# Performance work log

Hardware: AMD Instinct MI355X
Metric: run time of the kernel (lower is better)

The kernel has to match this reference:

```python
import jax, jax.numpy as jnp
import numpy as np

B, S, D, H = 4, 2048, 1024, 16
DEPTH = D // H


def setup_inputs() -> dict:
    key = jax.random.key(0)
    ks = jax.random.split(key, 12)
    q = jax.random.normal(ks[0], (B, S, D), dtype=jnp.float32)
    k = jax.random.normal(ks[1], (B, S, D), dtype=jnp.float32)
    v = jax.random.normal(ks[2], (B, S, D), dtype=jnp.float32)
    # causal mask: 1.0 where attention is disallowed (upper triangle), per `mask * -1e9`
    mask = 1.0 - jnp.tril(jnp.ones((S, S), dtype=jnp.float32))
    mask = mask[None, None, :, :]  # [1,1,S,S] broadcastable over batch/heads
    scale = 1.0 / np.sqrt(D)
    Wq = jax.random.normal(ks[3], (D, D), dtype=jnp.float32) * scale
    Wk = jax.random.normal(ks[4], (D, D), dtype=jnp.float32) * scale
    Wv = jax.random.normal(ks[5], (D, D), dtype=jnp.float32) * scale
    Wo = jax.random.normal(ks[6], (D, D), dtype=jnp.float32) * scale
    bq = jnp.zeros((D,), jnp.float32)
    bk = jnp.zeros((D,), jnp.float32)
    bv = jnp.zeros((D,), jnp.float32)
    bo = jnp.zeros((D,), jnp.float32)
    return {"query": q, "key": k, "value": v, "mask": mask,
            "Wq": Wq, "bq": bq, "Wk": Wk, "bk": bk,
            "Wv": Wv, "bv": bv, "Wo": Wo, "bo": bo}


def _split_heads(x):
    # [B, S, D] -> [B, H, S, depth]
    b, s, _ = x.shape
    return x.reshape(b, s, H, DEPTH).transpose(0, 2, 1, 3)


def reference(query, key, value, mask, Wq, bq, Wk, bk, Wv, bv, Wo, bo):
    q = _split_heads(query @ Wq + bq)   # [B,H,S,depth]
    k = _split_heads(key @ Wk + bk)
    v = _split_heads(value @ Wv + bv)
    scores = jnp.einsum('bhqd,bhkd->bhqk', q, k) / jnp.sqrt(
        jnp.asarray(DEPTH, q.dtype))
    scores = scores + mask * (-1e9)
    attn = jax.nn.softmax(scores, axis=-1)
    out = jnp.einsum('bhqk,bhkd->bhqd', attn, v)   # [B,H,S,depth]
    out = out.transpose(0, 2, 1, 3).reshape(query.shape[0], -1, H * DEPTH)
    return out @ Wo + bo
```

## Files before the change

kernel.cpp:

```cpp
#include <hip/hip_runtime.h>

#define Bsz 4
#define SEQ 2048
#define DIM 1024
#define NH 16
#define HD 64

typedef float  f32x4  __attribute__((ext_vector_type(4)));
typedef __bf16 bf16x8 __attribute__((ext_vector_type(8)));
typedef __bf16 bf16x4 __attribute__((ext_vector_type(4)));
typedef short  s16x4  __attribute__((ext_vector_type(4)));

__device__ __forceinline__ f32x4 mfma16(bf16x8 a, bf16x8 b, f32x4 c) {
    return __builtin_amdgcn_mfma_f32_16x16x32_bf16(a, b, c, 0, 0, 0);
}
__device__ __forceinline__ f32x4 mfma16k16(bf16x4 a, bf16x4 b, f32x4 c) {
#if defined(__has_builtin) && __has_builtin(__builtin_amdgcn_mfma_f32_16x16x16bf16_1k)
    return __builtin_amdgcn_mfma_f32_16x16x16bf16_1k(
        __builtin_bit_cast(s16x4, a), __builtin_bit_cast(s16x4, b), c, 0, 0, 0);
#else
    asm volatile("s_nop 2\n\tv_mfma_f32_16x16x16_bf16 %0, %1, %2, %0\n\ts_nop 7\n\ts_nop 7"
                 : "+v"(c) : "v"(a), "v"(b));
    return c;
#endif
}

#define GLD_LDS16(gsrc, ldst)                                                        \
    __builtin_amdgcn_global_load_lds(                                                \
        (const __attribute__((address_space(1))) void*)(gsrc),                       \
        (__attribute__((address_space(3))) void*)(ldst), 16, 0, 0)

__global__ __launch_bounds__(256) void cvt_kernel(
    const float* __restrict__ x0, const float* __restrict__ x1,
    const float* __restrict__ x2,
    __bf16* __restrict__ o0, __bf16* __restrict__ o1, __bf16* __restrict__ o2)
{
    int z = blockIdx.y;
    const float* X = (z == 0) ? x0 : (z == 1) ? x1 : x2;
    __bf16*      O = (z == 0) ? o0 : (z == 1) ? o1 : o2;
    size_t i = ((size_t)blockIdx.x * 256 + threadIdx.x) * 8;
    f32x4 a = *(const f32x4*)(X + i);
    f32x4 b = *(const f32x4*)(X + i + 4);
    bf16x8 r;
#pragma unroll
    for (int j = 0; j < 4; j++) { r[j] = (__bf16)a[j]; r[4 + j] = (__bf16)b[j]; }
    *(bf16x8*)(O + i) = r;
}

__global__ __launch_bounds__(256) void wt_kernel(
    const float* __restrict__ Wq, const float* __restrict__ Wk,
    const float* __restrict__ Wv, const float* __restrict__ Wo,
    __bf16* __restrict__ wt)
{
    __shared__ float tile[64][65];
    int z = blockIdx.z;
    const float* W = (z == 0) ? Wq : (z == 1) ? Wk : (z == 2) ? Wv : Wo;
    __bf16* out = wt + (size_t)z * DIM * DIM;
    int kb = blockIdx.x * 64, nb = blockIdx.y * 64;
    int t = threadIdx.x;
    int cidx = t & 63, ridx = t >> 6;
#pragma unroll
    for (int i = 0; i < 16; i++) {
        int r = ridx + i * 4;
        tile[r][cidx] = W[(size_t)(kb + r) * DIM + nb + cidx];
    }
    __syncthreads();
#pragma unroll
    for (int i = 0; i < 16; i++) {
        int r = ridx + i * 4;
        out[(size_t)(nb + r) * DIM + kb + cidx] = (__bf16)tile[cidx][r];
    }
}

__global__ __launch_bounds__(256, 2) void gemm_proj(
    const __bf16* __restrict__ Xq, const __bf16* __restrict__ Xk,
    const __bf16* __restrict__ Xv, const __bf16* __restrict__ wt,
    const float* __restrict__ bq, const float* __restrict__ bk,
    const float* __restrict__ bv,
    __bf16* __restrict__ oq, __bf16* __restrict__ ok, __bf16* __restrict__ ovT)
{
    int z = blockIdx.z;
    const __bf16* X    = (z == 0) ? Xq : (z == 1) ? Xk : Xv;
    const float*  bias = (z == 0) ? bq : (z == 1) ? bk : bv;
    const __bf16* Bt   = wt + (size_t)z * DIM * DIM;

    __shared__ __align__(16) char smem[32768];
    __bf16* const Ab = (__bf16*)smem;
    __bf16* const Bb = (__bf16*)(smem + 16384);

    int m0 = blockIdx.x * 128, n0 = blockIdx.y * 128;
    int tid = threadIdx.x, lane = tid & 63, w = tid >> 6;
    int c = lane & 15, g = lane >> 4;
    int wm = (w >> 1) * 64, wn = (w & 1) * 64;

    f32x4 acc[4][4] = {};

    int srow = (w * 2) * 16 + (lane >> 2);
    int scol = (lane & 3) * 8;
    const __bf16* aptr0 = X + (size_t)(m0 + srow) * DIM + scol;
    const __bf16* aptr1 = aptr0 + (size_t)16 * DIM;
    const __bf16* bptr0 = Bt + (size_t)(n0 + srow) * DIM + scol;
    const __bf16* bptr1 = bptr0 + (size_t)16 * DIM;
    int so0 = (w * 2) * 512;
    int so1 = (w * 2 + 1) * 512;

    GLD_LDS16(aptr0, Ab + so0);
    GLD_LDS16(aptr1, Ab + so1);
    GLD_LDS16(bptr0, Bb + so0);
    GLD_LDS16(bptr1, Bb + so1);
    __syncthreads();

    int cur = 0;
    for (int kt = 0; kt < 32; ++kt) {
        int nxt = kt + 1;
        int nb = cur ^ 1;
        if (nxt < 32) {
            int k0 = nxt * 32;
            GLD_LDS16(aptr0 + k0, Ab + nb * 4096 + so0);
            GLD_LDS16(aptr1 + k0, Ab + nb * 4096 + so1);
            GLD_LDS16(bptr0 + k0, Bb + nb * 4096 + so0);
            GLD_LDS16(bptr1 + k0, Bb + nb * 4096 + so1);
        }
        bf16x8 af[4], bf[4];
#pragma unroll
        for (int mf = 0; mf < 4; mf++)
            af[mf] = *(bf16x8*)&Ab[cur * 4096 + (wm + mf * 16 + c) * 32 + g * 8];
#pragma unroll
        for (int nf = 0; nf < 4; nf++)
            bf[nf] = *(bf16x8*)&Bb[cur * 4096 + (wn + nf * 16 + c) * 32 + g * 8];
#pragma unroll
        for (int mf = 0; mf < 4; mf++)
#pragma unroll
            for (int nf = 0; nf < 4; nf++)
                acc[mf][nf] = mfma16(af[mf], bf[nf], acc[mf][nf]);
        __syncthreads();
        cur = nb;
    }

    if (z == 2) {
        __bf16* T = (__bf16*)smem + (size_t)w * 2304;
        int h = (n0 + wn) >> 6;
        int bb = m0 >> 11;
        int s_base = (m0 & (SEQ - 1)) + wm;
        int dd = lane >> 2;
        int ss = (lane & 3) * 8;
        size_t obase = ((size_t)(bb * NH + h) * HD) * SEQ;
#pragma unroll
        for (int half = 0; half < 2; half++) {
#pragma unroll
            for (int mh = 0; mh < 2; mh++) {
                int mf = half * 2 + mh;
#pragma unroll
                for (int nf = 0; nf < 4; nf++) {
                    int col = n0 + wn + nf * 16 + c;
                    int d = nf * 16 + c;
                    float bval = bias[col];
                    bf16x4 pk;
#pragma unroll
                    for (int r = 0; r < 4; r++) pk[r] = (__bf16)(acc[mf][nf][r] + bval);
                    *(bf16x4*)&T[d * 36 + mh * 16 + g * 4] = pk;
                }
            }
#pragma unroll
            for (int dgrp = 0; dgrp < 4; dgrp++) {
                int d = dgrp * 16 + dd;
                bf16x8 vv = *(bf16x8*)&T[d * 36 + ss];
                *(bf16x8*)&ovT[obase + (size_t)d * SEQ + s_base + half * 32 + ss] = vv;
            }
        }
    } else {
        __bf16* Out = (z == 0) ? oq : ok;
#pragma unroll
        for (int nf = 0; nf < 4; nf++) {
            int col = n0 + wn + nf * 16 + c;
            float bval = bias[col];
#pragma unroll
            for (int mf = 0; mf < 4; mf++) {
                int row = m0 + wm + mf * 16 + g * 4;
#pragma unroll
                for (int r = 0; r < 4; r++)
                    Out[(size_t)(row + r) * DIM + col] = (__bf16)(acc[mf][nf][r] + bval);
            }
        }
    }
}

__global__ __launch_bounds__(256, 2) void gemm_proj_f32(
    const float* __restrict__ Xq, const float* __restrict__ Xk,
    const float* __restrict__ Xv, const __bf16* __restrict__ wt,
    const float* __restrict__ bq, const float* __restrict__ bk,
    const float* __restrict__ bv,
    __bf16* __restrict__ oq, __bf16* __restrict__ ok, __bf16* __restrict__ ovT)
{
    int z = blockIdx.z;
    const float*  X    = (z == 0) ? Xq : (z == 1) ? Xk : Xv;
    const float*  bias = (z == 0) ? bq : (z == 1) ? bk : bv;
    const __bf16* Bt   = wt + (size_t)z * DIM * DIM;

    __shared__ __align__(16) char smem[36864];
    __bf16* const Ab = (__bf16*)smem;
    __bf16* const Bb = (__bf16*)(smem + 16384);

    int m0 = blockIdx.x * 128, n0 = blockIdx.y * 128;
    int tid = threadIdx.x, lane = tid & 63, w = tid >> 6;
    int c = lane & 15, g = lane >> 4;
    int wm = (w >> 1) * 64, wn = (w & 1) * 64;

    f32x4 acc[4][4] = {};

    int ar = tid >> 1, ah = tid & 1;
    const float* aptr = X + (size_t)(m0 + ar) * DIM + ah * 16;
    int awo = ar * 32 + ah * 16;

    int brow0 = (w * 2) * 16 + (lane >> 2);
    int bcol  = (lane & 3) * 8;
    const __bf16* bptr0 = Bt + (size_t)(n0 + brow0) * DIM + bcol;
    const __bf16* bptr1 = bptr0 + (size_t)16 * DIM;
    int bwo0 = (w * 2) * 512;
    int bwo1 = (w * 2 + 1) * 512;

    {
        f32x4 f0 = *(const f32x4*)(aptr);
        f32x4 f1 = *(const f32x4*)(aptr + 4);
        f32x4 f2 = *(const f32x4*)(aptr + 8);
        f32x4 f3 = *(const f32x4*)(aptr + 12);
        GLD_LDS16(bptr0, Bb + bwo0);
        GLD_LDS16(bptr1, Bb + bwo1);
        bf16x8 b0, b1;
#pragma unroll
        for (int j = 0; j < 4; j++) {
            b0[j] = (__bf16)f0[j]; b0[4 + j] = (__bf16)f1[j];
            b1[j] = (__bf16)f2[j]; b1[4 + j] = (__bf16)f3[j];
        }
        *(bf16x8*)(Ab + awo)     = b0;
        *(bf16x8*)(Ab + awo + 8) = b1;
    }
    __syncthreads();

    int cur = 0;
    for (int kt = 0; kt < 32; ++kt) {
        int nxt = kt + 1;
        int nb = cur ^ 1;
        f32x4 f0, f1, f2, f3;
        if (nxt < 32) {
            const float* ap = aptr + nxt * 32;
            f0 = *(const f32x4*)(ap);
            f1 = *(const f32x4*)(ap + 4);
            f2 = *(const f32x4*)(ap + 8);
            f3 = *(const f32x4*)(ap + 12);
            GLD_LDS16(bptr0 + nxt * 32, Bb + nb * 4096 + bwo0);
            GLD_LDS16(bptr1 + nxt * 32, Bb + nb * 4096 + bwo1);
        }
        bf16x8 af[4], bf[4];
#pragma unroll
        for (int mf = 0; mf < 4; mf++)
            af[mf] = *(bf16x8*)&Ab[cur * 4096 + (wm + mf * 16 + c) * 32 + g * 8];
#pragma unroll
        for (int nf = 0; nf < 4; nf++)
            bf[nf] = *(bf16x8*)&Bb[cur * 4096 + (wn + nf * 16 + c) * 32 + g * 8];
#pragma unroll
        for (int mf = 0; mf < 4; mf++)
#pragma unroll
            for (int nf = 0; nf < 4; nf++)
                acc[mf][nf] = mfma16(af[mf], bf[nf], acc[mf][nf]);
        if (nxt < 32) {
            bf16x8 b0, b1;
#pragma unroll
            for (int j = 0; j < 4; j++) {
                b0[j] = (__bf16)f0[j]; b0[4 + j] = (__bf16)f1[j];
                b1[j] = (__bf16)f2[j]; b1[4 + j] = (__bf16)f3[j];
            }
            *(bf16x8*)(Ab + nb * 4096 + awo)     = b0;
            *(bf16x8*)(Ab + nb * 4096 + awo + 8) = b1;
        }
        __syncthreads();
        cur = nb;
    }

    if (z == 2) {
        __bf16* T = (__bf16*)smem + (size_t)w * 4608;
#pragma unroll
        for (int nf = 0; nf < 4; nf++) {
            int col = n0 + wn + nf * 16 + c;
            int d = nf * 16 + c;
            float bval = bias[col];
#pragma unroll
            for (int mf = 0; mf < 4; mf++) {
                int sl = mf * 16 + g * 4;
                bf16x4 pk;
#pragma unroll
                for (int r = 0; r < 4; r++) pk[r] = (__bf16)(acc[mf][nf][r] + bval);
                *(bf16x4*)&T[d * 72 + sl] = pk;
            }
        }
        int h = (n0 + wn) >> 6;
        int bb = m0 >> 11;
        int s_base = (m0 & (SEQ - 1)) + wm;
        int dd = lane >> 2;
        int ss = (lane & 3) * 8;
        size_t obase = ((size_t)(bb * NH + h) * HD) * SEQ;
#pragma unroll
        for (int dgrp = 0; dgrp < 4; dgrp++)
#pragma unroll
            for (int half = 0; half < 2; half++) {
                int d = dgrp * 16 + dd;
                int s = half * 32 + ss;
                bf16x8 vv = *(bf16x8*)&T[d * 72 + s];
                *(bf16x8*)&ovT[obase + (size_t)d * SEQ + s_base + s] = vv;
            }
    } else {
        __bf16* Out = (z == 0) ? oq : ok;
#pragma unroll
        for (int nf = 0; nf < 4; nf++) {
            int col = n0 + wn + nf * 16 + c;
            float bval = bias[col];
#pragma unroll
            for (int mf = 0; mf < 4; mf++) {
                int row = m0 + wm + mf * 16 + g * 4;
#pragma unroll
                for (int r = 0; r < 4; r++)
                    Out[(size_t)(row + r) * DIM + col] = (__bf16)(acc[mf][nf][r] + bval);
            }
        }
    }
}

#define QSCALE 0.180336880f

__global__ __launch_bounds__(256, 2) void fa_kernel(
    const __bf16* __restrict__ qp, const __bf16* __restrict__ kp,
    const __bf16* __restrict__ vpT, __bf16* __restrict__ op)
{
    int bz = blockIdx.x;
    int bh = bz & 63;
    int b = bh >> 4, h = bh & 15;
    int qt = 15 - (bz >> 6);
    int q0 = qt * 128;

    int tid = threadIdx.x, lane = tid & 63, w = tid >> 6;
    int c = lane & 15, g = lane >> 4;

    __shared__ __bf16 Kbuf[64 * 64];
    __shared__ __bf16 Vbuf[64 * 64];

    const int qb[2] = {q0 + w * 16, q0 + 64 + w * 16};

    bf16x8 qf[2][2];
#pragma unroll
    for (int nq = 0; nq < 2; nq++) {
        const __bf16* qbase = qp + (size_t)(b * SEQ + qb[nq] + c) * DIM + h * HD;
#pragma unroll
        for (int kc = 0; kc < 2; kc++) {
            bf16x8 raw = *(const bf16x8*)(qbase + kc * 32 + g * 8);
            bf16x8 sc;
#pragma unroll
            for (int j = 0; j < 8; j++) sc[j] = (__bf16)((float)raw[j] * QSCALE);
            qf[nq][kc] = sc;
        }
    }

    f32x4 acc[4][2] = {};
    float m_run[2] = {-1e30f, -1e30f};
    float l_run[2] = {0.f, 0.f};

    int r8 = tid >> 3, c8 = tid & 7;
    int sch = c8 ^ (r8 & 7);
    const __bf16* kbase = kp  + (size_t)(b * SEQ + r8) * DIM + h * HD + sch * 8;
    const __bf16* vbase = vpT + ((size_t)(b * NH + h) * HD + r8) * SEQ + sch * 8;
    __bf16* kdst0 = Kbuf + w * 512;
    __bf16* kdst1 = Kbuf + 2048 + w * 512;
    __bf16* vdst0 = Vbuf + w * 512;
    __bf16* vdst1 = Vbuf + 2048 + w * 512;

    int vb4[4];
#pragma unroll
    for (int mkey = 0; mkey < 4; mkey++)
        vb4[mkey] = c * 64 + (((2 * mkey + (g >> 1)) ^ (c & 7)) * 8) + (g & 1) * 4;

    int ktmax = (q0 >> 6) + 2;
    for (int kt = 0; kt < ktmax; ++kt) {
        GLD_LDS16(kbase + (size_t)kt * 64 * DIM, kdst0);
        GLD_LDS16(kbase + (size_t)(kt * 64 + 32) * DIM, kdst1);
        GLD_LDS16(vbase + kt * 64, vdst0);
        GLD_LDS16(vbase + kt * 64 + (size_t)32 * SEQ, vdst1);
        __syncthreads();

        bool need0 = (kt * 64 <= qb[0] + 15);
        int kb0 = kt * 64;

        f32x4 s[4][2] = {};
#pragma unroll
        for (int kc = 0; kc < 2; kc++) {
            bf16x8 kf[4];
#pragma unroll
            for (int mkey = 0; mkey < 4; mkey++)
                kf[mkey] = *(bf16x8*)&Kbuf[(mkey * 16 + c) * 64 + (((kc * 4 + g) ^ (c & 7)) * 8)];
#pragma unroll
            for (int mkey = 0; mkey < 4; mkey++) {
                if (need0) s[mkey][0] = mfma16(kf[mkey], qf[0][kc], s[mkey][0]);
                s[mkey][1] = mfma16(kf[mkey], qf[1][kc], s[mkey][1]);
            }
        }

        bf16x4 pf[4][2];
#pragma unroll
        for (int nq = 0; nq < 2; nq++) {
            if (nq == 0 && !need0) continue;
            int qg = qb[nq] + c;
            if (kb0 + 63 > qg) {
#pragma unroll
                for (int mkey = 0; mkey < 4; mkey++)
#pragma unroll
                    for (int r2 = 0; r2 < 4; r2++)
                        if (kb0 + mkey * 16 + g * 4 + r2 > qg) s[mkey][nq][r2] = -1e30f;
            }
            float pm0 = fmaxf(fmaxf(s[0][nq][0], s[0][nq][1]), fmaxf(s[0][nq][2], s[0][nq][3]));
            float pm1 = fmaxf(fmaxf(s[1][nq][0], s[1][nq][1]), fmaxf(s[1][nq][2], s[1][nq][3]));
            float pm2 = fmaxf(fmaxf(s[2][nq][0], s[2][nq][1]), fmaxf(s[2][nq][2], s[2][nq][3]));
            float pm3 = fmaxf(fmaxf(s[3][nq][0], s[3][nq][1]), fmaxf(s[3][nq][2], s[3][nq][3]));
            float pm = fmaxf(fmaxf(pm0, pm1), fmaxf(pm2, pm3));
            pm = fmaxf(pm, __shfl_xor(pm, 16));
            pm = fmaxf(pm, __shfl_xor(pm, 32));
            float mo = m_run[nq];
            float mn = fmaxf(mo, pm);
            m_run[nq] = mn;
            float scl = exp2f(mo - mn);
            l_run[nq] *= scl;
#pragma unroll
            for (int nf = 0; nf < 4; nf++) acc[nf][nq] *= scl;
            float rs = 0.f;
#pragma unroll
            for (int mkey = 0; mkey < 4; mkey++) {
                bf16x4 pk;
#pragma unroll
                for (int r2 = 0; r2 < 4; r2++) {
                    float p = exp2f(s[mkey][nq][r2] - mn);
                    rs += p;
                    pk[r2] = (__bf16)p;
                }
                pf[mkey][nq] = pk;
            }
            rs += __shfl_xor(rs, 16);
            rs += __shfl_xor(rs, 32);
            l_run[nq] += rs;
        }

#pragma unroll
        for (int mkey = 0; mkey < 4; mkey++) {
#pragma unroll
            for (int nf = 0; nf < 4; nf++) {
                bf16x4 vf = *(bf16x4*)&Vbuf[vb4[mkey] + nf * 1024];
                if (need0) acc[nf][0] = mfma16k16(vf, pf[mkey][0], acc[nf][0]);
                acc[nf][1] = mfma16k16(vf, pf[mkey][1], acc[nf][1]);
            }
        }
        __syncthreads();
    }

#pragma unroll
    for (int nq = 0; nq < 2; nq++) {
        float inv = 1.f / l_run[nq];
        int row = qb[nq] + c;
        __bf16* obase = op + (size_t)(b * SEQ + row) * DIM + h * HD + g * 4;
#pragma unroll
        for (int nf = 0; nf < 4; nf++) {
            bf16x4 pk;
#pragma unroll
            for (int r2 = 0; r2 < 4; r2++) pk[r2] = (__bf16)(acc[nf][nq][r2] * inv);
            *(bf16x4*)(obase + nf * 16) = pk;
        }
    }
}

__global__ __launch_bounds__(256, 2) void gemm_out(
    const __bf16* __restrict__ Ain, const __bf16* __restrict__ wt,
    const float* __restrict__ bias, float* __restrict__ Out)
{
    const __bf16* Bt = wt + (size_t)3 * DIM * DIM;

    __shared__ __bf16 Ab[2][4096];
    __shared__ __bf16 Bb[2][4096];

    int m0 = blockIdx.x * 128, n0 = blockIdx.y * 128;
    int tid = threadIdx.x, lane = tid & 63, w = tid >> 6;
    int c = lane & 15, g = lane >> 4;
    int wm = (w >> 1) * 64, wn = (w & 1) * 64;

    f32x4 acc[4][4] = {};

    int srow = (w * 2) * 16 + (lane >> 2);
    int scol = (lane & 3) * 8;
    const __bf16* aptr0 = Ain + (size_t)(m0 + srow) * DIM + scol;
    const __bf16* aptr1 = aptr0 + (size_t)16 * DIM;
    const __bf16* bptr0 = Bt + (size_t)(n0 + srow) * DIM + scol;
    const __bf16* bptr1 = bptr0 + (size_t)16 * DIM;
    int so0 = (w * 2) * 512;
    int so1 = (w * 2 + 1) * 512;

    GLD_LDS16(aptr0, Ab[0] + so0);
    GLD_LDS16(aptr1, Ab[0] + so1);
    GLD_LDS16(bptr0, Bb[0] + so0);
    GLD_LDS16(bptr1, Bb[0] + so1);
    __syncthreads();

    int cur = 0;
    for (int kt = 0; kt < 32; ++kt) {
        int nxt = kt + 1;
        int nb = cur ^ 1;
        if (nxt < 32) {
            int k0 = nxt * 32;
            GLD_LDS16(aptr0 + k0, Ab[nb] + so0);
            GLD_LDS16(aptr1 + k0, Ab[nb] + so1);
            GLD_LDS16(bptr0 + k0, Bb[nb] + so0);
            GLD_LDS16(bptr1 + k0, Bb[nb] + so1);
        }
        bf16x8 af[4], bf[4];
#pragma unroll
        for (int mf = 0; mf < 4; mf++)
            af[mf] = *(bf16x8*)&Ab[cur][(wm + mf * 16 + c) * 32 + g * 8];
#pragma unroll
        for (int nf = 0; nf < 4; nf++)
            bf[nf] = *(bf16x8*)&Bb[cur][(wn + nf * 16 + c) * 32 + g * 8];
#pragma unroll
        for (int mf = 0; mf < 4; mf++)
#pragma unroll
            for (int nf = 0; nf < 4; nf++)
                acc[mf][nf] = mfma16(af[mf], bf[nf], acc[mf][nf]);
        __syncthreads();
        cur = nb;
    }

#pragma unroll
    for (int nf = 0; nf < 4; nf++) {
        int col = n0 + wn + nf * 16 + c;
        float bval = bias[col];
#pragma unroll
        for (int mf = 0; mf < 4; mf++) {
            int row = m0 + wm + mf * 16 + g * 4;
#pragma unroll
            for (int r = 0; r < 4; r++)
                Out[(size_t)(row + r) * DIM + col] = acc[mf][nf][r] + bval;
        }
    }
}

extern "C" void kernel_launch(void* const* d_in, const int* in_sizes, int n_in,
                              void* d_out, int out_size, void* d_ws, size_t ws_size,
                              hipStream_t stream)
{
    const float* q  = (const float*)d_in[0];
    const float* k  = (const float*)d_in[1];
    const float* v  = (const float*)d_in[2];
    const float* Wq = (const float*)d_in[4];
    const float* bq = (const float*)d_in[5];
    const float* Wk = (const float*)d_in[6];
    const float* bk = (const float*)d_in[7];
    const float* Wv = (const float*)d_in[8];
    const float* bv = (const float*)d_in[9];
    const float* Wo = (const float*)d_in[10];
    const float* bo = (const float*)d_in[11];

    char* ws = (char*)d_ws;
    __bf16* wt  = (__bf16*)ws;
    __bf16* qp  = (__bf16*)(ws + (size_t)(8u  << 20));
    __bf16* kp  = (__bf16*)(ws + (size_t)(24u << 20));
    __bf16* vpT = (__bf16*)(ws + (size_t)(40u << 20));
    __bf16* ao  = (__bf16*)(ws + (size_t)(56u << 20));
    __bf16* xq  = (__bf16*)(ws + (size_t)(72u << 20));
    __bf16* xk  = (__bf16*)(ws + (size_t)(88u << 20));
    __bf16* xv  = (__bf16*)(ws + (size_t)(104u << 20));

    wt_kernel<<<dim3(16, 16, 4), 256, 0, stream>>>(Wq, Wk, Wv, Wo, wt);
    if (ws_size >= ((size_t)120u << 20)) {
        cvt_kernel<<<dim3(4096, 3), 256, 0, stream>>>(q, k, v, xq, xk, xv);
        gemm_proj<<<dim3(64, 8, 3), 256, 0, stream>>>(xq, xk, xv, wt, bq, bk, bv, qp, kp, vpT);
    } else {
        gemm_proj_f32<<<dim3(64, 8, 3), 256, 0, stream>>>(q, k, v, wt, bq, bk, bv, qp, kp, vpT);
    }
    fa_kernel<<<dim3(1024), 256, 0, stream>>>(qp, kp, vpT, ao);
    gemm_out<<<dim3(64, 8), 256, 0, stream>>>(ao, wt, bo, (float*)d_out);

    (void)in_sizes; (void)n_in; (void)out_size;
}
```

Baseline: 203.5 us.

## Halve flash-attention query tile to 64 rows and add lazy softmax rescaling

Each attention block now handles 64 query rows (one 16-row strip per wave) instead of 128, and the grid doubles to 2048 blocks. This gives more parallelism and finer causal load balance, and drops the need0 branching, at the cost of loading each K/V tile twice as often per query row. It also adds a lazy rescale: the running max and accumulator rescale are updated only when some lane's new max exceeds the old one by more than 8 in log2 space. That skips exp and multiply work on most iterations, but it lets unnormalised probabilities grow up to 2^8.

```diff
diff --git a/kernel.cpp b/kernel.cpp
--- a/kernel.cpp
+++ b/kernel.cpp
@@ -334,8 +334,8 @@
     int bz = blockIdx.x;
     int bh = bz & 63;
     int b = bh >> 4, h = bh & 15;
-    int qt = 15 - (bz >> 6);
-    int q0 = qt * 128;
+    int qt = 31 - (bz >> 6);
+    int q0 = qt * 64;
 
     int tid = threadIdx.x, lane = tid & 63, w = tid >> 6;
     int c = lane & 15, g = lane >> 4;
@@ -343,25 +343,25 @@
     __shared__ __bf16 Kbuf[64 * 64];
     __shared__ __bf16 Vbuf[64 * 64];
 
-    const int qb[2] = {q0 + w * 16, q0 + 64 + w * 16};
-
-    bf16x8 qf[2][2];
-#pragma unroll
-    for (int nq = 0; nq < 2; nq++) {
-        const __bf16* qbase = qp + (size_t)(b * SEQ + qb[nq] + c) * DIM + h * HD;
+    const int qb = q0 + w * 16;
+    const int qg = qb + c;
+
+    bf16x8 qf[2];
+    {
+        const __bf16* qbase = qp + (size_t)(b * SEQ + qg) * DIM + h * HD;
 #pragma unroll
         for (int kc = 0; kc < 2; kc++) {
             bf16x8 raw = *(const bf16x8*)(qbase + kc * 32 + g * 8);
             bf16x8 sc;
 #pragma unroll
             for (int j = 0; j < 8; j++) sc[j] = (__bf16)((float)raw[j] * QSCALE);
-            qf[nq][kc] = sc;
-        }
-    }
-
-    f32x4 acc[4][2] = {};
-    float m_run[2] = {-1e30f, -1e30f};
-    float l_run[2] = {0.f, 0.f};
+            qf[kc] = sc;
+        }
+    }
+
+    f32x4 acc[4] = {};
+    float m_run = -1e30f;
+    float l_run = 0.f;
 
     int r8 = tid >> 3, c8 = tid & 7;
     int sch = c8 ^ (r8 & 7);
@@ -377,7 +377,7 @@
     for (int mkey = 0; mkey < 4; mkey++)
         vb4[mkey] = c * 64 + (((2 * mkey + (g >> 1)) ^ (c & 7)) * 8) + (g & 1) * 4;
 
-    int ktmax = (q0 >> 6) + 2;
+    int ktmax = qt + 1;
     for (int kt = 0; kt < ktmax; ++kt) {
         GLD_LDS16(kbase + (size_t)kt * 64 * DIM, kdst0);
         GLD_LDS16(kbase + (size_t)(kt * 64 + 32) * DIM, kdst1);
@@ -385,10 +385,9 @@
         GLD_LDS16(vbase + kt * 64 + (size_t)32 * SEQ, vdst1);
         __syncthreads();
 
-        bool need0 = (kt * 64 <= qb[0] + 15);
         int kb0 = kt * 64;
 
-        f32x4 s[4][2] = {};
+        f32x4 s[4] = {};
 #pragma unroll
         for (int kc = 0; kc < 2; kc++) {
             bf16x8 kf[4];
@@ -396,77 +395,69 @@
             for (int mkey = 0; mkey < 4; mkey++)
                 kf[mkey] = *(bf16x8*)&Kbuf[(mkey * 16 + c) * 64 + (((kc * 4 + g) ^ (c & 7)) * 8)];
 #pragma unroll
-            for (int mkey = 0; mkey < 4; mkey++) {
-                if (need0) s[mkey][0] = mfma16(kf[mkey], qf[0][kc], s[mkey][0]);
-                s[mkey][1] = mfma16(kf[mkey], qf[1][kc], s[mkey][1]);
-            }
-        }
-
-        bf16x4 pf[4][2];
-#pragma unroll
-        for (int nq = 0; nq < 2; nq++) {
-            if (nq == 0 && !need0) continue;
-            int qg = qb[nq] + c;
-            if (kb0 + 63 > qg) {
-#pragma unroll
-                for (int mkey = 0; mkey < 4; mkey++)
-#pragma unroll
-                    for (int r2 = 0; r2 < 4; r2++)
-                        if (kb0 + mkey * 16 + g * 4 + r2 > qg) s[mkey][nq][r2] = -1e30f;
-            }
-            float pm0 = fmaxf(fmaxf(s[0][nq][0], s[0][nq][1]), fmaxf(s[0][nq][2], s[0][nq][3]));
-            float pm1 = fmaxf(fmaxf(s[1][nq][0], s[1][nq][1]), fmaxf(s[1][nq][2], s[1][nq][3]));
-            float pm2 = fmaxf(fmaxf(s[2][nq][0], s[2][nq][1]), fmaxf(s[2][nq][2], s[2][nq][3]));
-            float pm3 = fmaxf(fmaxf(s[3][nq][0], s[3][nq][1]), fmaxf(s[3][nq][2], s[3][nq][3]));
-            float pm = fmaxf(fmaxf(pm0, pm1), fmaxf(pm2, pm3));
-            pm = fmaxf(pm, __shfl_xor(pm, 16));
-            pm = fmaxf(pm, __shfl_xor(pm, 32));
-            float mo = m_run[nq];
-            float mn = fmaxf(mo, pm);
-            m_run[nq] = mn;
-            float scl = exp2f(mo - mn);
-            l_run[nq] *= scl;
-#pragma unroll
-            for (int nf = 0; nf < 4; nf++) acc[nf][nq] *= scl;
-            float rs = 0.f;
-#pragma unroll
-            for (int mkey = 0; mkey < 4; mkey++) {
-                bf16x4 pk;
-#pragma unroll
-                for (int r2 = 0; r2 < 4; r2++) {
-                    float p = exp2f(s[mkey][nq][r2] - mn);
-                    rs += p;
-                    pk[r2] = (__bf16)p;
-                }
-                pf[mkey][nq] = pk;
-            }
-            rs += __shfl_xor(rs, 16);
-            rs += __shfl_xor(rs, 32);
-            l_run[nq] += rs;
-        }
+            for (int mkey = 0; mkey < 4; mkey++)
+                s[mkey] = mfma16(kf[mkey], qf[kc], s[mkey]);
+        }
+
+        if (kb0 + 63 > qg) {
+#pragma unroll
+            for (int mkey = 0; mkey < 4; mkey++)
+#pragma unroll
+                for (int r2 = 0; r2 < 4; r2++)
+                    if (kb0 + mkey * 16 + g * 4 + r2 > qg) s[mkey][r2] = -1e30f;
+        }
+
+        float pm0 = fmaxf(fmaxf(s[0][0], s[0][1]), fmaxf(s[0][2], s[0][3]));
+        float pm1 = fmaxf(fmaxf(s[1][0], s[1][1]), fmaxf(s[1][2], s[1][3]));
+        float pm2 = fmaxf(fmaxf(s[2][0], s[2][1]), fmaxf(s[2][2], s[2][3]));
+        float pm3 = fmaxf(fmaxf(s[3][0], s[3][1]), fmaxf(s[3][2], s[3][3]));
+        float pm = fmaxf(fmaxf(pm0, pm1), fmaxf(pm2, pm3));
+        pm = fmaxf(pm, __shfl_xor(pm, 16));
+        pm = fmaxf(pm, __shfl_xor(pm, 32));
+        if (!__all(pm <= m_run + 8.f)) {
+            float mn = fmaxf(m_run, pm);
+            float scl = exp2f(m_run - mn);
+            l_run *= scl;
+#pragma unroll
+            for (int nf = 0; nf < 4; nf++) acc[nf] *= scl;
+            m_run = mn;
+        }
+        float rs = 0.f;
+        bf16x4 pf[4];
+#pragma unroll
+        for (int mkey = 0; mkey < 4; mkey++) {
+            bf16x4 pk;
+#pragma unroll
+            for (int r2 = 0; r2 < 4; r2++) {
+                float p = exp2f(s[mkey][r2] - m_run);
+                rs += p;
+                pk[r2] = (__bf16)p;
+            }
+            pf[mkey] = pk;
+        }
+        rs += __shfl_xor(rs, 16);
+        rs += __shfl_xor(rs, 32);
+        l_run += rs;
 
 #pragma unroll
         for (int mkey = 0; mkey < 4; mkey++) {
 #pragma unroll
             for (int nf = 0; nf < 4; nf++) {
                 bf16x4 vf = *(bf16x4*)&Vbuf[vb4[mkey] + nf * 1024];
-                if (need0) acc[nf][0] = mfma16k16(vf, pf[mkey][0], acc[nf][0]);
-                acc[nf][1] = mfma16k16(vf, pf[mkey][1], acc[nf][1]);
+                acc[nf] = mfma16k16(vf, pf[mkey], acc[nf]);
             }
         }
         __syncthreads();
     }
 
-#pragma unroll
-    for (int nq = 0; nq < 2; nq++) {
-        float inv = 1.f / l_run[nq];
-        int row = qb[nq] + c;
-        __bf16* obase = op + (size_t)(b * SEQ + row) * DIM + h * HD + g * 4;
+    {
+        float inv = 1.f / l_run;
+        __bf16* obase = op + (size_t)(b * SEQ + qg) * DIM + h * HD + g * 4;
 #pragma unroll
         for (int nf = 0; nf < 4; nf++) {
             bf16x4 pk;
 #pragma unroll
-            for (int r2 = 0; r2 < 4; r2++) pk[r2] = (__bf16)(acc[nf][nq][r2] * inv);
+            for (int r2 = 0; r2 < 4; r2++) pk[r2] = (__bf16)(acc[nf][r2] * inv);
             *(bf16x4*)(obase + nf * 16) = pk;
         }
     }
@@ -577,7 +568,7 @@
     } else {
         gemm_proj_f32<<<dim3(64, 8, 3), 256, 0, stream>>>(q, k, v, wt, bq, bk, bv, qp, kp, vpT);
     }
-    fa_kernel<<<dim3(1024), 256, 0, stream>>>(qp, kp, vpT, ao);
+    fa_kernel<<<dim3(2048), 256, 0, stream>>>(qp, kp, vpT, ao);
     gemm_out<<<dim3(64, 8), 256, 0, stream>>>(ao, wt, bo, (float*)d_out);
 
     (void)in_sizes; (void)n_in; (void)out_size;
```

After: 196.2 us. -3.6%, faster.
